# Kernel tuning notes

Measured on AMD Instinct MI355X. Metric: run time of the kernel, lower is better.

The kernel has to match this reference:

```python
import jax, jax.numpy as jnp
import numpy as np

N_NODES = 50000
N_EDGES = 800000
D_IN = 128
D_HID = 128
N_CLS = 47


def setup_inputs() -> dict:
    key = jax.random.key(0)
    ks = jax.random.split(key, 10)
    inp = {
        "features": jax.random.normal(ks[0], (N_NODES, D_IN), dtype=jnp.float32),
        "src": jax.random.randint(ks[1], (N_EDGES,), 0, N_NODES),
        "dst": jax.random.randint(ks[2], (N_EDGES,), 0, N_NODES),
        "Wself0": jax.random.normal(ks[3], (D_IN, D_HID), dtype=jnp.float32) / np.sqrt(D_IN),
        "Wneigh0": jax.random.normal(ks[4], (D_IN, D_HID), dtype=jnp.float32) / np.sqrt(D_IN),
        "b0": jnp.zeros((D_HID,), dtype=jnp.float32),
        "Wself1": jax.random.normal(ks[5], (D_HID, D_HID), dtype=jnp.float32) / np.sqrt(D_HID),
        "Wneigh1": jax.random.normal(ks[6], (D_HID, D_HID), dtype=jnp.float32) / np.sqrt(D_HID),
        "b1": jnp.zeros((D_HID,), dtype=jnp.float32),
        "Wself2": jax.random.normal(ks[7], (D_HID, N_CLS), dtype=jnp.float32) / np.sqrt(D_HID),
        "Wneigh2": jax.random.normal(ks[8], (D_HID, N_CLS), dtype=jnp.float32) / np.sqrt(D_HID),
        "b2": jnp.zeros((N_CLS,), dtype=jnp.float32),
    }
    return inp


def reference(features, src, dst, Wself0, Wneigh0, b0, Wself1, Wneigh1, b1, Wself2, Wneigh2, b2):
    # GraphSAGE (DGL SAGEConv, aggregator_type='mean', eval mode so dropout is identity).
    # Per layer: h_neigh[v] = mean_{(u->v) in E} h[u]; out = h @ W_self + h_neigh @ W_neigh + b
    n = features.shape[0]
    # in-degree for mean aggregation (zero-degree nodes get zero neighbor feature)
    deg = jax.ops.segment_sum(jnp.ones(dst.shape, dtype=features.dtype), dst, num_segments=n)
    inv_deg = (1.0 / jnp.maximum(deg, 1.0))[:, None]  # [N,1]

    def sage_layer(h, Ws, Wn, b, act):
        # gather src features per edge, scatter-add into dst, normalize by in-degree
        agg = jax.ops.segment_sum(h[src], dst, num_segments=n) * inv_deg  # [N, d]
        out = h @ Ws + agg @ Wn + b
        return jax.nn.relu(out) if act else out

    h = sage_layer(features, Wself0, Wneigh0, b0, True)
    h = sage_layer(h, Wself1, Wneigh1, b1, True)
    h = sage_layer(h, Wself2, Wneigh2, b2, False)
    return h
```

## Files before the change

kernel.cpp:

```cpp
#include <hip/hip_runtime.h>

#define D 128
#define NCLS 47

typedef short short8 __attribute__((ext_vector_type(8)));
typedef float floatx4 __attribute__((ext_vector_type(4)));

typedef __attribute__((address_space(3))) unsigned int lds_uint;
typedef const __attribute__((address_space(1))) unsigned int glb_uint;

__device__ __forceinline__ float bf16lo(unsigned int u) {
    union { unsigned int i; float f; } c; c.i = u << 16; return c.f;
}
__device__ __forceinline__ float bf16hi(unsigned int u) {
    union { unsigned int i; float f; } c; c.i = u & 0xffff0000u; return c.f;
}
__device__ __forceinline__ unsigned short f2bf(float f) {
    union { float f; unsigned int i; } c; c.f = f;
    unsigned int r = c.i + 0x7fffu + ((c.i >> 16) & 1u);
    return (unsigned short)(r >> 16);
}
__device__ __forceinline__ unsigned int pack2(float x, float y) {
    return (unsigned int)f2bf(x) | ((unsigned int)f2bf(y) << 16);
}

__device__ __forceinline__ void gload_lds16(const unsigned int* g, unsigned int* l) {
    __builtin_amdgcn_global_load_lds((glb_uint*)g, (lds_uint*)l, 16, 0, 0);
}
#define WAITVM0 asm volatile("s_waitcnt vmcnt(0)" ::: "memory")
#define WAITVM1 asm volatile("s_waitcnt vmcnt(1)" ::: "memory")

#define FBm 1024
__global__ __launch_bounds__(256) void fill_prep_kernel(
    const int* __restrict__ src, const int* __restrict__ dst,
    int* __restrict__ cnt0, int* __restrict__ cnt1,
    unsigned short* __restrict__ csr, int n_edges,
    const float* __restrict__ f, unsigned int* __restrict__ hA,
    unsigned int* __restrict__ hBz, int npairs, int n,
    const float* __restrict__ Ws0, const float* __restrict__ Wn0, unsigned short* __restrict__ Wt0,
    const float* __restrict__ Ws1, const float* __restrict__ Wn1, unsigned short* __restrict__ Wt1,
    const float* __restrict__ Ws2, const float* __restrict__ Wn2, unsigned short* __restrict__ Wt2) {
    if (blockIdx.x < FBm) {
        int cohort = blockIdx.x & 7;
        int cb = blockIdx.x >> 3;
        int nth = (FBm >> 3) * 256;
        int tid = cb * 256 + threadIdx.x;
        int range = (n + 7) >> 3;
        int lo = cohort * range;
        int hi = lo + range;
        if (hi > n) hi = n;
        const int4* dst4 = (const int4*)dst;
        int nq = n_edges >> 2;
        for (int q = tid; q < nq; q += nth) {
            int4 dd = dst4[q];
            int e = q << 2;
            if (dd.x >= lo && dd.x < hi) {
                int p = atomicAdd(&cnt0[dd.x], 1);
                if (p < 32) csr[dd.x * 64 + p] = (unsigned short)src[e];
            }
            if (dd.y >= lo && dd.y < hi) {
                int p = atomicAdd(&cnt1[dd.y], 1);
                if (p < 32) csr[dd.y * 64 + 32 + p] = (unsigned short)src[e + 1];
            }
            if (dd.z >= lo && dd.z < hi) {
                int p = atomicAdd(&cnt0[dd.z], 1);
                if (p < 32) csr[dd.z * 64 + p] = (unsigned short)src[e + 2];
            }
            if (dd.w >= lo && dd.w < hi) {
                int p = atomicAdd(&cnt1[dd.w], 1);
                if (p < 32) csr[dd.w * 64 + 32 + p] = (unsigned short)src[e + 3];
            }
        }
        for (int e = (nq << 2) + tid; e < n_edges; e += nth) {
            int d = dst[e];
            if (d >= lo && d < hi) {
                if (e & 1) {
                    int p = atomicAdd(&cnt1[d], 1);
                    if (p < 32) csr[d * 64 + 32 + p] = (unsigned short)src[e];
                } else {
                    int p = atomicAdd(&cnt0[d], 1);
                    if (p < 32) csr[d * 64 + p] = (unsigned short)src[e];
                }
            }
        }
        return;
    }
    int tid = (blockIdx.x - FBm) * 256 + threadIdx.x;
    int stride = (gridDim.x - FBm) * 256;
    int total = npairs + 2 * 128 * 256 + 64 * 256 + 64;
    for (int gid = tid; gid < total; gid += stride) {
        if (gid < npairs) {
            if (gid < npairs - 64) {
                float2 v = ((const float2*)f)[gid];
                hA[gid] = pack2(v.x, v.y);
            } else {
                hA[gid] = 0u;
            }
            continue;
        }
        int r = gid - npairs;
        if (r < 128 * 256) {
            int nn = r >> 8, k = r & 255;
            float v = (k < 128) ? Ws0[k * 128 + nn] : Wn0[(k - 128) * 128 + nn];
            Wt0[nn * 256 + k] = f2bf(v);
            continue;
        }
        r -= 128 * 256;
        if (r < 128 * 256) {
            int nn = r >> 8, k = r & 255;
            float v = (k < 128) ? Ws1[k * 128 + nn] : Wn1[(k - 128) * 128 + nn];
            Wt1[nn * 256 + k] = f2bf(v);
            continue;
        }
        r -= 128 * 256;
        if (r < 64 * 256) {
            int nn = r >> 8, k = r & 255;
            float v = 0.0f;
            if (nn < NCLS) v = (k < 128) ? Ws2[k * NCLS + nn] : Wn2[(k - 128) * NCLS + nn];
            Wt2[nn * 256 + k] = f2bf(v);
            continue;
        }
        r -= 64 * 256;
        if (r < 64) hBz[(size_t)n * 64 + r] = 0u;
    }
}

__global__ __launch_bounds__(256, 8) void sage_fused_kernel(
    const unsigned int* __restrict__ hself,
    const unsigned int* __restrict__ hagg,
    const unsigned short* __restrict__ csr,
    const int* __restrict__ cnt0,
    const int* __restrict__ cnt1,
    const unsigned short* __restrict__ Wt,
    const float* __restrict__ bias,
    unsigned short* __restrict__ hout,
    float* __restrict__ out,
    int n, int mode) {
    __shared__ unsigned int selfl[16][68];
    __shared__ unsigned int aggl[16][68];
    __shared__ __align__(16) unsigned short idxl[16][64];
    __shared__ int dl[16];
    __shared__ unsigned int sbuf[4][512];

    int wave = threadIdx.x >> 6;
    int lane = threadIdx.x & 63;
    int base = blockIdx.x * 16;
    const uint4* hs4 = (const uint4*)hself;

    {
        int rowi = threadIdx.x >> 4;
        int q = threadIdx.x & 15;
        int ns = base + rowi;
        unsigned sent = (unsigned)n;
        uint4 sv; sv.x = 0u; sv.y = 0u; sv.z = 0u; sv.w = 0u;
        int c0 = 0, c1 = 0;
        if (ns < n) {
            sv = hs4[(size_t)ns * 16 + q];
            c0 = cnt0[ns]; if (c0 > 32) c0 = 32;
            c1 = cnt1[ns]; if (c1 > 32) c1 = 32;
        }
        *(uint4*)&selfl[rowi][q * 4] = sv;
        int d = c0 + c1;
        const unsigned short* crow = csr + (size_t)ns * 64;
        int j = q * 4;
        unsigned e0 = (j     < d) ? (unsigned)crow[j     < c0 ? j     : 32 + j     - c0] : sent;
        unsigned e1 = (j + 1 < d) ? (unsigned)crow[j + 1 < c0 ? j + 1 : 32 + j + 1 - c0] : sent;
        unsigned e2 = (j + 2 < d) ? (unsigned)crow[j + 2 < c0 ? j + 2 : 32 + j + 2 - c0] : sent;
        unsigned e3 = (j + 3 < d) ? (unsigned)crow[j + 3 < c0 ? j + 3 : 32 + j + 3 - c0] : sent;
        unsigned int* ip = (unsigned int*)&idxl[rowi][0];
        ip[q * 2]     = e0 | (e1 << 16);
        ip[q * 2 + 1] = e2 | (e3 << 16);
        if (q == 0) dl[rowi] = d;
    }
    __syncthreads();

    unsigned int* sbw = &sbuf[wave][0];

    if (mode == 1) {
        int l4 = (lane >> 4);
        int lc = (lane & 15) * 4;
        for (int i = 0; i < 4; ++i) {
            int li = wave * 4 + i;
            int d = dl[li];
            int nst = (d + 3) >> 2;
            float ax = 0.f, ay = 0.f;
            if (nst > 0) {
                {
                    unsigned ridx = idxl[li][l4];
                    gload_lds16(hagg + (size_t)ridx * 64 + lc, sbw);
                }
                for (int s = 1; s < nst; ++s) {
                    unsigned ridx = idxl[li][s * 4 + l4];
                    gload_lds16(hagg + (size_t)ridx * 64 + lc, sbw + (s & 1) * 256);
                    WAITVM1;
                    const unsigned int* sp = sbw + ((s - 1) & 1) * 256 + lane;
#pragma unroll
                    for (int j = 0; j < 4; ++j) {
                        unsigned u = sp[j * 64];
                        ax += bf16lo(u); ay += bf16hi(u);
                    }
                }
                WAITVM0;
                const unsigned int* sp = sbw + ((nst - 1) & 1) * 256 + lane;
#pragma unroll
                for (int j = 0; j < 4; ++j) {
                    unsigned u = sp[j * 64];
                    ax += bf16lo(u); ay += bf16hi(u);
                }
            }
            float inv = 1.0f / fmaxf((float)d, 1.0f);
            aggl[li][lane] = pack2(ax * inv, ay * inv);
        }
    } else {
        int l8 = (lane >> 3);
        int lc = (lane & 7) * 4;
        int col = lane & 31;
        int half = lane >> 5;
        for (int i = 0; i < 4; ++i) {
            int li = wave * 4 + i;
            int d = dl[li];
            int nst = (d + 7) >> 3;
            float ax = 0.f, ay = 0.f;
            if (nst > 0) {
                {
                    unsigned ridx = idxl[li][l8];
                    gload_lds16(hagg + (size_t)ridx * 32 + lc, sbw);
                }
                for (int s = 1; s < nst; ++s) {
                    unsigned ridx = idxl[li][s * 8 + l8];
                    gload_lds16(hagg + (size_t)ridx * 32 + lc, sbw + (s & 1) * 256);
                    WAITVM1;
                    const unsigned int* sp = sbw + ((s - 1) & 1) * 256 + half * 128 + col;
#pragma unroll
                    for (int j = 0; j < 4; ++j) {
                        unsigned u = sp[j * 32];
                        ax += bf16lo(u); ay += bf16hi(u);
                    }
                }
                WAITVM0;
                const unsigned int* sp = sbw + ((nst - 1) & 1) * 256 + half * 128 + col;
#pragma unroll
                for (int j = 0; j < 4; ++j) {
                    unsigned u = sp[j * 32];
                    ax += bf16lo(u); ay += bf16hi(u);
                }
            }
            ax += __shfl_xor(ax, 32, 64);
            ay += __shfl_xor(ay, 32, 64);
            if (half == 0) {
                float inv = 1.0f / fmaxf((float)d, 1.0f);
                float* fr = (float*)&aggl[li][0];
                fr[2 * col] = ax * inv;
                fr[2 * col + 1] = ay * inv;
            }
        }
    }
    __syncthreads();

    int m = lane & 15;
    int quad = lane >> 4;
    const unsigned short* arow = (const unsigned short*)&selfl[m][0];

    if (mode == 1) {
        const unsigned short* lrow = (const unsigned short*)&aggl[m][0];
        int t0 = wave * 2;
        floatx4 acc[2];
        acc[0] = (floatx4){0.f, 0.f, 0.f, 0.f};
        acc[1] = (floatx4){0.f, 0.f, 0.f, 0.f};
#pragma unroll
        for (int ko = 0; ko < 128; ko += 32) {
            short8 av = *(const short8*)(arow + ko + quad * 8);
#pragma unroll
            for (int tt = 0; tt < 2; ++tt) {
                short8 bfr = *(const short8*)(Wt + (size_t)((t0 + tt) * 16 + m) * 256 + ko + quad * 8);
                acc[tt] = __builtin_amdgcn_mfma_f32_16x16x32_bf16(av, bfr, acc[tt], 0, 0, 0);
            }
        }
#pragma unroll
        for (int ko = 0; ko < 128; ko += 32) {
            short8 av = *(const short8*)(lrow + ko + quad * 8);
#pragma unroll
            for (int tt = 0; tt < 2; ++tt) {
                short8 bfr = *(const short8*)(Wt + (size_t)((t0 + tt) * 16 + m) * 256 + 128 + ko + quad * 8);
                acc[tt] = __builtin_amdgcn_mfma_f32_16x16x32_bf16(av, bfr, acc[tt], 0, 0, 0);
            }
        }
#pragma unroll
        for (int tt = 0; tt < 2; ++tt) {
            int nfeat = (t0 + tt) * 16 + m;
            float bb = bias[nfeat];
#pragma unroll
            for (int r = 0; r < 4; ++r) {
                int node = base + quad * 4 + r;
                if (node < n) {
                    float v = fmaxf(acc[tt][r] + bb, 0.0f);
                    hout[(size_t)node * 128 + nfeat] = f2bf(v);
                }
            }
        }
    } else {
        if (wave < 3) {
            floatx4 acc = (floatx4){0.f, 0.f, 0.f, 0.f};
#pragma unroll
            for (int ko = 0; ko < 128; ko += 32) {
                short8 av = *(const short8*)(arow + ko + quad * 8);
                short8 bfr = *(const short8*)(Wt + (size_t)(wave * 16 + m) * 256 + ko + quad * 8);
                acc = __builtin_amdgcn_mfma_f32_16x16x32_bf16(av, bfr, acc, 0, 0, 0);
            }
            int nfeat = wave * 16 + m;
            if (nfeat < NCLS) {
                float bb = bias[nfeat];
#pragma unroll
                for (int r = 0; r < 4; ++r) {
                    int node = base + quad * 4 + r;
                    if (node < n) {
                        const float* fr = (const float*)&aggl[quad * 4 + r][0];
                        out[(size_t)node * NCLS + nfeat] = acc[r] + fr[nfeat] + bb;
                    }
                }
            }
        }
    }
}

__global__ __launch_bounds__(256) void proj_kernel(
    const unsigned int* __restrict__ hin,
    const unsigned short* __restrict__ Wt,
    unsigned short* __restrict__ P,
    int np) {
    __shared__ unsigned int sl[16][68];
    int wave = threadIdx.x >> 6;
    int lane = threadIdx.x & 63;
    int pb = blockIdx.x * 16;
    const uint4* h4 = (const uint4*)hin;
    {
        int rowi = threadIdx.x >> 4;
        int q = threadIdx.x & 15;
        int ns = pb + rowi;
        uint4 sv; sv.x = 0u; sv.y = 0u; sv.z = 0u; sv.w = 0u;
        if (ns < np) sv = h4[(size_t)ns * 16 + q];
        *(uint4*)&sl[rowi][q * 4] = sv;
    }
    __syncthreads();
    int m = lane & 15;
    int quad = lane >> 4;
    const unsigned short* arow = (const unsigned short*)&sl[m][0];
    floatx4 acc = (floatx4){0.f, 0.f, 0.f, 0.f};
#pragma unroll
    for (int ko = 0; ko < 128; ko += 32) {
        short8 av = *(const short8*)(arow + ko + quad * 8);
        short8 bfr = *(const short8*)(Wt + (size_t)(wave * 16 + m) * 256 + 128 + ko + quad * 8);
        acc = __builtin_amdgcn_mfma_f32_16x16x32_bf16(av, bfr, acc, 0, 0, 0);
    }
    int col = wave * 16 + m;
#pragma unroll
    for (int r = 0; r < 4; ++r) {
        int node = pb + quad * 4 + r;
        if (node < np) P[(size_t)node * 64 + col] = f2bf(acc[r]);
    }
}

extern "C" void kernel_launch(void* const* d_in, const int* in_sizes, int n_in,
                              void* d_out, int out_size, void* d_ws, size_t ws_size,
                              hipStream_t stream) {
    const float* features = (const float*)d_in[0];
    const int* src = (const int*)d_in[1];
    const int* dst = (const int*)d_in[2];
    const float* Ws0 = (const float*)d_in[3];
    const float* Wn0 = (const float*)d_in[4];
    const float* b0 = (const float*)d_in[5];
    const float* Ws1 = (const float*)d_in[6];
    const float* Wn1 = (const float*)d_in[7];
    const float* b1 = (const float*)d_in[8];
    const float* Ws2 = (const float*)d_in[9];
    const float* Wn2 = (const float*)d_in[10];
    const float* b2 = (const float*)d_in[11];
    float* out = (float*)d_out;

    int n = in_sizes[0] / D;
    int n_edges = in_sizes[1];
    int np1 = n + 1;

    int* cnt0 = (int*)d_ws;
    int* cnt1 = cnt0 + 50048;
    unsigned short* csr = (unsigned short*)(cnt1 + 50048);
    unsigned int* hA = (unsigned int*)(csr + (size_t)n * 64 + 32);
    unsigned int* hB = hA + (size_t)np1 * 64;
    unsigned short* Wt0 = (unsigned short*)(hB + (size_t)np1 * 64);
    unsigned short* Wt1 = Wt0 + 128 * 256;
    unsigned short* Wt2 = Wt1 + 128 * 256;
    unsigned short* P = (unsigned short*)(Wt2 + 64 * 256);

    int npairs = np1 * 64;

    hipMemsetAsync(cnt0, 0, (size_t)2 * 50048 * sizeof(int), stream);
    fill_prep_kernel<<<2048, 256, 0, stream>>>(
        src, dst, cnt0, cnt1, csr, n_edges, features, hA, hB, npairs, n,
        Ws0, Wn0, Wt0, Ws1, Wn1, Wt1, Ws2, Wn2, Wt2);

    int tiles = (n + 15) / 16;

    sage_fused_kernel<<<tiles, 256, 0, stream>>>(hA, hA, csr, cnt0, cnt1, Wt0, b0,
                                                 (unsigned short*)hB, nullptr, n, 1);
    sage_fused_kernel<<<tiles, 256, 0, stream>>>(hB, hB, csr, cnt0, cnt1, Wt1, b1,
                                                 (unsigned short*)hA, nullptr, n, 1);
    proj_kernel<<<(np1 + 15) / 16, 256, 0, stream>>>(hA, Wt2, P, np1);
    sage_fused_kernel<<<tiles, 256, 0, stream>>>(hA, (const unsigned int*)P, csr, cnt0, cnt1,
                                                 Wt2, b2, nullptr, out, n, 2);
}
```

Baseline: 282.4 us.

## Fuse final-layer neighbor projection into second SAGE layer epilogue

Removes the standalone projection kernel. The second layer's fused kernel now stages its ReLU output tile in shared memory and immediately multiplies it by the third layer's neighbor weights, writing the projected P buffer. This avoids a launch and a full re-read of the hidden activations. The prep kernel is also restructured so all blocks perform both CSR fill and conversion work, and it zeroes P's padding row. The trade-off is extra barriers and MFMA work in the layer-2 epilogue.

```diff
diff --git a/kernel.cpp b/kernel.cpp
--- a/kernel.cpp
+++ b/kernel.cpp
@@ -30,20 +30,20 @@
 #define WAITVM0 asm volatile("s_waitcnt vmcnt(0)" ::: "memory")
 #define WAITVM1 asm volatile("s_waitcnt vmcnt(1)" ::: "memory")
 
-#define FBm 1024
 __global__ __launch_bounds__(256) void fill_prep_kernel(
     const int* __restrict__ src, const int* __restrict__ dst,
     int* __restrict__ cnt0, int* __restrict__ cnt1,
     unsigned short* __restrict__ csr, int n_edges,
     const float* __restrict__ f, unsigned int* __restrict__ hA,
-    unsigned int* __restrict__ hBz, int npairs, int n,
+    unsigned int* __restrict__ hBz, unsigned int* __restrict__ Pz,
+    int npairs, int n,
     const float* __restrict__ Ws0, const float* __restrict__ Wn0, unsigned short* __restrict__ Wt0,
     const float* __restrict__ Ws1, const float* __restrict__ Wn1, unsigned short* __restrict__ Wt1,
     const float* __restrict__ Ws2, const float* __restrict__ Wn2, unsigned short* __restrict__ Wt2) {
-    if (blockIdx.x < FBm) {
+    {
         int cohort = blockIdx.x & 7;
         int cb = blockIdx.x >> 3;
-        int nth = (FBm >> 3) * 256;
+        int nth = (gridDim.x >> 3) * 256;
         int tid = cb * 256 + threadIdx.x;
         int range = (n + 7) >> 3;
         int lo = cohort * range;
@@ -83,11 +83,10 @@
                 }
             }
         }
-        return;
     }
-    int tid = (blockIdx.x - FBm) * 256 + threadIdx.x;
-    int stride = (gridDim.x - FBm) * 256;
-    int total = npairs + 2 * 128 * 256 + 64 * 256 + 64;
+    int tid = blockIdx.x * 256 + threadIdx.x;
+    int stride = gridDim.x * 256;
+    int total = npairs + 2 * 128 * 256 + 64 * 256 + 64 + 32;
     for (int gid = tid; gid < total; gid += stride) {
         if (gid < npairs) {
             if (gid < npairs - 64) {
@@ -121,7 +120,9 @@
             continue;
         }
         r -= 64 * 256;
-        if (r < 64) hBz[(size_t)n * 64 + r] = 0u;
+        if (r < 64) { hBz[(size_t)n * 64 + r] = 0u; continue; }
+        r -= 64;
+        if (r < 32) Pz[(size_t)n * 32 + r] = 0u;
     }
 }
 
@@ -135,6 +136,8 @@
     const float* __restrict__ bias,
     unsigned short* __restrict__ hout,
     float* __restrict__ out,
+    const unsigned short* __restrict__ WtP,
+    unsigned short* __restrict__ Pout,
     int n, int mode) {
     __shared__ unsigned int selfl[16][68];
     __shared__ unsigned int aggl[16][68];
@@ -285,6 +288,7 @@
                 acc[tt] = __builtin_amdgcn_mfma_f32_16x16x32_bf16(av, bfr, acc[tt], 0, 0, 0);
             }
         }
+        float vout[2][4];
 #pragma unroll
         for (int tt = 0; tt < 2; ++tt) {
             int nfeat = (t0 + tt) * 16 + m;
@@ -292,10 +296,36 @@
 #pragma unroll
             for (int r = 0; r < 4; ++r) {
                 int node = base + quad * 4 + r;
-                if (node < n) {
-                    float v = fmaxf(acc[tt][r] + bb, 0.0f);
-                    hout[(size_t)node * 128 + nfeat] = f2bf(v);
-                }
+                float v = fmaxf(acc[tt][r] + bb, 0.0f);
+                vout[tt][r] = v;
+                if (node < n) hout[(size_t)node * 128 + nfeat] = f2bf(v);
+            }
+        }
+
+        if (Pout) {
+            __syncthreads();
+            unsigned short* hl = (unsigned short*)&selfl[0][0];
+#pragma unroll
+            for (int tt = 0; tt < 2; ++tt) {
+                int nfeat = (t0 + tt) * 16 + m;
+#pragma unroll
+                for (int r = 0; r < 4; ++r) {
+                    hl[(quad * 4 + r) * 136 + nfeat] = f2bf(vout[tt][r]);
+                }
+            }
+            __syncthreads();
+            floatx4 pacc = (floatx4){0.f, 0.f, 0.f, 0.f};
+#pragma unroll
+            for (int ko = 0; ko < 128; ko += 32) {
+                short8 av = *(const short8*)(hl + m * 136 + ko + quad * 8);
+                short8 bfr = *(const short8*)(WtP + (size_t)(wave * 16 + m) * 256 + 128 + ko + quad * 8);
+                pacc = __builtin_amdgcn_mfma_f32_16x16x32_bf16(av, bfr, pacc, 0, 0, 0);
+            }
+            int pcol = wave * 16 + m;
+#pragma unroll
+            for (int r = 0; r < 4; ++r) {
+                int node = base + quad * 4 + r;
+                if (node < n) Pout[(size_t)node * 64 + pcol] = f2bf(pacc[r]);
             }
         }
     } else {
@@ -320,43 +350,6 @@
                 }
             }
         }
-    }
-}
-
-__global__ __launch_bounds__(256) void proj_kernel(
-    const unsigned int* __restrict__ hin,
-    const unsigned short* __restrict__ Wt,
-    unsigned short* __restrict__ P,
-    int np) {
-    __shared__ unsigned int sl[16][68];
-    int wave = threadIdx.x >> 6;
-    int lane = threadIdx.x & 63;
-    int pb = blockIdx.x * 16;
-    const uint4* h4 = (const uint4*)hin;
-    {
-        int rowi = threadIdx.x >> 4;
-        int q = threadIdx.x & 15;
-        int ns = pb + rowi;
-        uint4 sv; sv.x = 0u; sv.y = 0u; sv.z = 0u; sv.w = 0u;
-        if (ns < np) sv = h4[(size_t)ns * 16 + q];
-        *(uint4*)&sl[rowi][q * 4] = sv;
-    }
-    __syncthreads();
-    int m = lane & 15;
-    int quad = lane >> 4;
-    const unsigned short* arow = (const unsigned short*)&sl[m][0];
-    floatx4 acc = (floatx4){0.f, 0.f, 0.f, 0.f};
-#pragma unroll
-    for (int ko = 0; ko < 128; ko += 32) {
-        short8 av = *(const short8*)(arow + ko + quad * 8);
-        short8 bfr = *(const short8*)(Wt + (size_t)(wave * 16 + m) * 256 + 128 + ko + quad * 8);
-        acc = __builtin_amdgcn_mfma_f32_16x16x32_bf16(av, bfr, acc, 0, 0, 0);
-    }
-    int col = wave * 16 + m;
-#pragma unroll
-    for (int r = 0; r < 4; ++r) {
-        int node = pb + quad * 4 + r;
-        if (node < np) P[(size_t)node * 64 + col] = f2bf(acc[r]);
     }
 }
 
@@ -395,16 +388,19 @@
 
     hipMemsetAsync(cnt0, 0, (size_t)2 * 50048 * sizeof(int), stream);
     fill_prep_kernel<<<2048, 256, 0, stream>>>(
-        src, dst, cnt0, cnt1, csr, n_edges, features, hA, hB, npairs, n,
+        src, dst, cnt0, cnt1, csr, n_edges, features, hA, hB, (unsigned int*)P,
+        npairs, n,
         Ws0, Wn0, Wt0, Ws1, Wn1, Wt1, Ws2, Wn2, Wt2);
 
     int tiles = (n + 15) / 16;
 
     sage_fused_kernel<<<tiles, 256, 0, stream>>>(hA, hA, csr, cnt0, cnt1, Wt0, b0,
-                                                 (unsigned short*)hB, nullptr, n, 1);
+                                                 (unsigned short*)hB, nullptr,
+                                                 nullptr, nullptr, n, 1);
     sage_fused_kernel<<<tiles, 256, 0, stream>>>(hB, hB, csr, cnt0, cnt1, Wt1, b1,
-                                                 (unsigned short*)hA, nullptr, n, 1);
-    proj_kernel<<<(np1 + 15) / 16, 256, 0, stream>>>(hA, Wt2, P, np1);
+                                                 (unsigned short*)hA, nullptr,
+                                                 Wt2, P, n, 1);
     sage_fused_kernel<<<tiles, 256, 0, stream>>>(hA, (const unsigned int*)P, csr, cnt0, cnt1,
-                                                 Wt2, b2, nullptr, out, n, 2);
-}
+                                                 Wt2, b2, nullptr, out,
+                                                 nullptr, nullptr, n, 2);
+}
```

Measured after the change: 278.3 us. No clear change (-1.5%).
